# Performance work log

Measured on AMD Instinct MI355X. Metric: run time of the kernel, lower is better.

## Reference

```python
import jax, jax.numpy as jnp
import numpy as np
import math

N, B, S = 2048, 4, 1024
SFZ, IFZ, H, A = 384, 256, 8, 64
LN_EPS = 1e-5


def setup_inputs() -> dict:
    key = jax.random.key(0)
    ks = jax.random.split(key, 12)
    x = jax.random.normal(ks[0], (N, IFZ), dtype=jnp.float32)
    emb = jax.random.normal(ks[1], (B, S, SFZ), dtype=jnp.float32)
    mask = jax.random.randint(ks[2], (B, S), 0, 2).astype(bool)
    batch = jnp.sort(jax.random.randint(ks[3], (N,), 0, B)).astype(jnp.int64)
    sc = 1.0 / math.sqrt(IFZ)
    scs = 1.0 / math.sqrt(SFZ)
    Wq = jax.random.normal(ks[4], (IFZ, H * A), dtype=jnp.float32) * sc
    Wk = jax.random.normal(ks[5], (SFZ, H * A), dtype=jnp.float32) * scs
    Wv = jax.random.normal(ks[6], (SFZ, H * A), dtype=jnp.float32) * scs
    Wg = jax.random.normal(ks[7], (IFZ, H * A), dtype=jnp.float32) * sc
    bg = jnp.zeros((H * A,), dtype=jnp.float32)
    Wback = jax.random.normal(ks[8], (H * A, IFZ), dtype=jnp.float32) / math.sqrt(H * A)
    bback = jnp.zeros((IFZ,), dtype=jnp.float32)
    gamma = jnp.ones((IFZ,), dtype=jnp.float32)
    beta = jnp.zeros((IFZ,), dtype=jnp.float32)
    return {"x": x, "packed_sequence_emb": emb, "packed_sequence_mask": mask,
            "batch": batch, "Wq": Wq, "Wk": Wk, "Wv": Wv, "Wg": Wg, "bg": bg,
            "Wback": Wback, "bback": bback, "gamma": gamma, "beta": beta}


def _masked_softmax(scores, mask):
    # scores: [N,S,H], mask: [N,S,1] bool; softmax over S with padded entries zeroed
    neg = jnp.finfo(scores.dtype).min
    s = jnp.where(mask, scores, neg)
    s = s - jnp.max(s, axis=1, keepdims=True)
    e = jnp.exp(s) * mask
    return e / (jnp.sum(e, axis=1, keepdims=True) + 1e-9)


def reference(x, packed_sequence_emb, packed_sequence_mask, batch,
              Wq, Wk, Wv, Wg, bg, Wback, bback, gamma, beta):
    scale = math.sqrt(A)
    q = (x @ Wq).reshape(N, H, A)                               # [N,H,A]
    k = (packed_sequence_emb @ Wk).reshape(B, S, H, A)          # [B,S,H,A]
    v = (packed_sequence_emb @ Wv).reshape(B, S, H, A)
    # scores per (node, candidate-batch), then gather node's own batch entry;
    # avoids materializing k[batch] of shape [N,S,H,A]
    scores_all = jnp.einsum('nha,bsha->nbsh', q, k) / scale     # [N,B,S,H]
    idx = batch[:, None, None, None].astype(jnp.int32)
    scores = jnp.take_along_axis(scores_all, idx, axis=1)[:, 0]  # [N,S,H]
    bmask = packed_sequence_mask[batch][..., None]               # [N,S,1]
    w = _masked_softmax(scores, bmask)                           # [N,S,H]
    feat_all = jnp.einsum('nsh,bsha->nbha', w, v)                # [N,B,H,A]
    feat = jnp.take_along_axis(feat_all, idx, axis=1)[:, 0]      # [N,H,A]
    gate = jax.nn.sigmoid(x @ Wg + bg).reshape(N, H, A)
    new = (gate * feat).reshape(N, H * A) @ Wback + bback        # [N,IFZ]
    y = math.sqrt(2.0) * x + new
    mu = jnp.mean(y, axis=-1, keepdims=True)
    var = jnp.mean((y - mu) ** 2, axis=-1, keepdims=True)
    out = (y - mu) * jax.lax.rsqrt(var + LN_EPS) * gamma + beta
    seq_aa_logits = jnp.sum(scores[..., :2], axis=-1)            # [N,S]
    return out, seq_aa_logits
```

## Files before the change

### kernel.cpp

```cpp
#include <hip/hip_runtime.h>
#include <hip/hip_bf16.h>

#define NND 2048
#define BBATCH 4
#define SS 1024
#define SFZ 384
#define IFZ 256
#define HH 8
#define AA 64
#define HA 512
#define ABLK 12
#define NGRP 4
#define NSPL 8

typedef __attribute__((ext_vector_type(8))) short bf16x8;
typedef __attribute__((ext_vector_type(4))) float f32x4;
typedef __attribute__((ext_vector_type(2))) unsigned int u32x2;

__device__ __forceinline__ unsigned short f2bf(float f) {
    union { float f; unsigned u; } a; a.f = f;
    unsigned r = a.u + 0x7fffu + ((a.u >> 16) & 1u);
    return (unsigned short)(r >> 16);
}
__device__ __forceinline__ float bf2f(unsigned short u) {
    return __uint_as_float((unsigned)u << 16);
}

__device__ __forceinline__ bf16x8 cvt8(const float* __restrict__ p) {
    const float4 f0 = *(const float4*)p;
    const float4 f1 = *(const float4*)(p + 4);
    bf16x8 o;
    o[0] = (short)f2bf(f0.x); o[1] = (short)f2bf(f0.y);
    o[2] = (short)f2bf(f0.z); o[3] = (short)f2bf(f0.w);
    o[4] = (short)f2bf(f1.x); o[5] = (short)f2bf(f1.y);
    o[6] = (short)f2bf(f1.z); o[7] = (short)f2bf(f1.w);
    return o;
}

__device__ __forceinline__ bf16x8 gld16(const unsigned short* p) {
    bf16x8 r;
    asm volatile("global_load_dwordx4 %0, %1, off" : "=&v"(r) : "v"(p));
    return r;
}
__device__ __forceinline__ f32x4 gldf4(const float* p) {
    f32x4 r;
    asm volatile("global_load_dwordx4 %0, %1, off" : "=&v"(r) : "v"(p));
    return r;
}
__device__ __forceinline__ u32x2 gld8(const unsigned short* p) {
    u32x2 r;
    asm volatile("global_load_dwordx2 %0, %1, off" : "=&v"(r) : "v"(p));
    return r;
}
#define VMWAIT0() do { \
    asm volatile("s_waitcnt vmcnt(0)" ::: "memory"); \
    __builtin_amdgcn_sched_barrier(0); \
} while (0)

__device__ __forceinline__ void tile_transpose(
    const float* __restrict__ src, unsigned short* __restrict__ dst,
    int K, int N, int kt, int nt, int t)
{
    __shared__ unsigned short tile[64][65];
    const int k0 = kt * 64, n0 = nt * 64;
    const int tr = t >> 6, tc = t & 63;
    #pragma unroll
    for (int r = 0; r < 16; ++r)
        tile[tr + r*4][tc] = f2bf(src[(size_t)(k0 + tr + r*4) * N + n0 + tc]);
    __syncthreads();
    #pragma unroll
    for (int r = 0; r < 16; ++r)
        dst[(size_t)(n0 + tr + r*4) * K + k0 + tc] = tile[tc][tr + r*4];
}

__global__ __launch_bounds__(256) void prep_kernel(
    const float* __restrict__ Wk, const float* __restrict__ Wv,
    const float* __restrict__ Wq, const float* __restrict__ Wg,
    const float* __restrict__ Wback,
    const void* __restrict__ mask_raw, const void* __restrict__ batch_raw,
    unsigned short* __restrict__ WkT, unsigned short* __restrict__ WvT,
    unsigned short* __restrict__ WqT, unsigned short* __restrict__ WgT,
    unsigned short* __restrict__ WbackT,
    float* __restrict__ mask_f, int* __restrict__ seg)
{
    const int bx = blockIdx.x, t = threadIdx.x;
    if (bx < 48)  { tile_transpose(Wk, WkT, SFZ, HA, bx/8, bx%8, t); return; }
    if (bx < 96)  { const int i = bx-48;  tile_transpose(Wv, WvT, SFZ, HA, i/8, i%8, t); return; }
    if (bx < 128) { const int i = bx-96;  tile_transpose(Wq, WqT, IFZ, HA, i/8, i%8, t); return; }
    if (bx < 160) { const int i = bx-128; tile_transpose(Wg, WgT, IFZ, HA, i/8, i%8, t); return; }
    if (bx < 192) { const int i = bx-160; tile_transpose(Wback, WbackT, HA, IFZ, i/4, i%4, t); return; }
    __shared__ int fl[4];
    __shared__ int fb;
    __shared__ int cnt[4];
    if (t < 4) { fl[t] = 0; cnt[t] = 0; }
    if (t == 0) fb = 0;
    __syncthreads();
    const unsigned char*  mb = (const unsigned char*)mask_raw;
    const unsigned short* mh = (const unsigned short*)mask_raw;
    const unsigned int*   mw = (const unsigned int*)mask_raw;
    int f0 = 0, f1 = 0, f2 = 0, f3 = 0;
    for (int i = t; i < 2048; i += 256) {
        unsigned short h = mh[i];
        if (h == 0x3f80u) f0 = 1;
        if ((i & 1) == 0 && h != 0) f1 = 1;
    }
    for (int i = t; i < 4096; i += 256)
        if ((i & 3) != 0 && mb[i] != 0) f2 = 1;
    for (int i = t; i < 1024; i += 256)
        if ((i & 1) != 0 && mw[i] != 0) f3 = 1;
    const int* bw = (const int*)batch_raw;
    int f4 = 0;
    for (int i = t + 1; i < 2048; i += 256)
        if (bw[i] < bw[i-1]) f4 = 1;
    if (f0) atomicOr(&fl[0], 1);
    if (f1) atomicOr(&fl[1], 1);
    if (f2) atomicOr(&fl[2], 1);
    if (f3) atomicOr(&fl[3], 1);
    if (f4) atomicOr(&fb, 1);
    __syncthreads();
    int mode;
    if (fl[0])      mode = fl[1] ? 1 : 0;
    else if (fl[2]) mode = 2;
    else if (fl[3]) mode = 3;
    else            mode = 4;
    for (int s = t; s < BBATCH*SS; s += 256) {
        int m;
        switch (mode) {
            case 0:  m = (mw[s]   != 0); break;
            case 1:  m = (mh[s]   != 0); break;
            case 2:  m = (mb[s]   != 0); break;
            case 3:  m = (mw[s]   != 0); break;
            default: m = (mw[2*s] != 0); break;
        }
        mask_f[s] = m ? 1.0f : 0.0f;
    }
    const int b64 = fb;
    for (int i = t; i < NND; i += 256) {
        const int bv = (b64 ? bw[2*i] : bw[i]) & 3;
        atomicAdd(&cnt[bv], 1);
    }
    __syncthreads();
    if (t == 0) {
        int s = 0;
        for (int b = 0; b < 4; ++b) { seg[2*b] = s; s += cnt[b]; seg[2*b+1] = s; }
    }
}

__global__ __launch_bounds__(256, 2) void proj_mfma(
    const float* __restrict__ emb, const float* __restrict__ x,
    const unsigned short* __restrict__ WkT, const unsigned short* __restrict__ WvT,
    const unsigned short* __restrict__ WqT, const unsigned short* __restrict__ WgT,
    const float* __restrict__ bg,
    unsigned short* __restrict__ k_blk, unsigned short* __restrict__ vT_bf,
    unsigned short* __restrict__ q_bf, float* __restrict__ gate_ws)
{
    __shared__ unsigned short v_l[16][520];
    const int t = threadIdx.x, w = t >> 6, lane = t & 63;
    const int m16 = lane & 15, quad = lane >> 4;
    const int bx = blockIdx.x;
    if (bx < 256) {
        const int r0 = bx * 16;
        const int b = r0 >> 10, srow = r0 & (SS - 1);
        const float* ap = emb + (size_t)(r0 + m16) * SFZ + quad * 8;
        bf16x8 af[12];
        #pragma unroll
        for (int j = 0; j < 12; ++j) af[j] = cvt8(ap + j * 32);
        #pragma unroll
        for (int tensor = 0; tensor < 2; ++tensor) {
            const unsigned short* Wt = tensor ? WvT : WkT;
            #pragma unroll
            for (int g = 0; g < 2; ++g) {
                const int n0g = w * 128 + g * 64;
                const unsigned short* bp0 = Wt + (size_t)(n0g +  0 + m16) * SFZ + quad * 8;
                const unsigned short* bp1 = Wt + (size_t)(n0g + 16 + m16) * SFZ + quad * 8;
                const unsigned short* bp2 = Wt + (size_t)(n0g + 32 + m16) * SFZ + quad * 8;
                const unsigned short* bp3 = Wt + (size_t)(n0g + 48 + m16) * SFZ + quad * 8;
                f32x4 a0 = (f32x4){0.f, 0.f, 0.f, 0.f};
                f32x4 a1 = a0, a2 = a0, a3 = a0;
                bf16x8 wb[24];
                #pragma unroll
                for (int j = 0; j < 6; ++j) {
                    wb[j*4+0] = gld16(bp0 + j * 32);
                    wb[j*4+1] = gld16(bp1 + j * 32);
                    wb[j*4+2] = gld16(bp2 + j * 32);
                    wb[j*4+3] = gld16(bp3 + j * 32);
                }
                VMWAIT0();
                #pragma unroll
                for (int j = 0; j < 6; ++j) {
                    a0 = __builtin_amdgcn_mfma_f32_16x16x32_bf16(af[j], wb[j*4+0], a0, 0, 0, 0);
                    a1 = __builtin_amdgcn_mfma_f32_16x16x32_bf16(af[j], wb[j*4+1], a1, 0, 0, 0);
                    a2 = __builtin_amdgcn_mfma_f32_16x16x32_bf16(af[j], wb[j*4+2], a2, 0, 0, 0);
                    a3 = __builtin_amdgcn_mfma_f32_16x16x32_bf16(af[j], wb[j*4+3], a3, 0, 0, 0);
                }
                #pragma unroll
                for (int j = 6; j < 12; ++j) {
                    wb[(j-6)*4+0] = gld16(bp0 + j * 32);
                    wb[(j-6)*4+1] = gld16(bp1 + j * 32);
                    wb[(j-6)*4+2] = gld16(bp2 + j * 32);
                    wb[(j-6)*4+3] = gld16(bp3 + j * 32);
                }
                VMWAIT0();
                #pragma unroll
                for (int j = 6; j < 12; ++j) {
                    a0 = __builtin_amdgcn_mfma_f32_16x16x32_bf16(af[j], wb[(j-6)*4+0], a0, 0, 0, 0);
                    a1 = __builtin_amdgcn_mfma_f32_16x16x32_bf16(af[j], wb[(j-6)*4+1], a1, 0, 0, 0);
                    a2 = __builtin_amdgcn_mfma_f32_16x16x32_bf16(af[j], wb[(j-6)*4+2], a2, 0, 0, 0);
                    a3 = __builtin_amdgcn_mfma_f32_16x16x32_bf16(af[j], wb[(j-6)*4+3], a3, 0, 0, 0);
                }
                f32x4 dd[4] = {a0, a1, a2, a3};
                if (tensor == 0) {
                    #pragma unroll
                    for (int u = 0; u < 4; ++u) {
                        const int n0 = n0g + u * 16;
                        const int head = n0 >> 6, coff = (n0 & 63) + m16;
                        unsigned short* kb = k_blk + (((size_t)(b * HH + head)) * SS) * 64 + coff;
                        #pragma unroll
                        for (int r = 0; r < 4; ++r)
                            kb[(size_t)(srow + quad * 4 + r) * 64] = f2bf(dd[u][r]);
                    }
                } else {
                    #pragma unroll
                    for (int u = 0; u < 4; ++u) {
                        const int c0 = n0g + u * 16 + m16;
                        #pragma unroll
                        for (int r = 0; r < 4; ++r)
                            v_l[quad * 4 + r][c0] = f2bf(dd[u][r]);
                    }
                }
            }
        }
        __syncthreads();
        for (int c = t; c < HA; c += 256) {
            unsigned short tmp[16];
            #pragma unroll
            for (int s = 0; s < 16; ++s) tmp[s] = v_l[s][c];
            unsigned short* dst = vT_bf + ((size_t)b * HA + c) * SS + srow;
            *(uint4*)dst       = ((const uint4*)tmp)[0];
            *(uint4*)(dst + 8) = ((const uint4*)tmp)[1];
        }
    } else {
        const int i = bx - 256;
        const int r0 = (i >> 1) * 16;
        const int half = i & 1;
        const float* ap = x + (size_t)(r0 + m16) * IFZ + quad * 8;
        bf16x8 af[8];
        #pragma unroll
        for (int j = 0; j < 8; ++j) af[j] = cvt8(ap + j * 32);
        const int n0b = half * 256 + w * 64;
        #pragma unroll
        for (int tensor = 0; tensor < 2; ++tensor) {
            const unsigned short* Wt = tensor ? WgT : WqT;
            const unsigned short* bp0 = Wt + (size_t)(n0b +  0 + m16) * IFZ + quad * 8;
            const unsigned short* bp1 = Wt + (size_t)(n0b + 16 + m16) * IFZ + quad * 8;
            const unsigned short* bp2 = Wt + (size_t)(n0b + 32 + m16) * IFZ + quad * 8;
            const unsigned short* bp3 = Wt + (size_t)(n0b + 48 + m16) * IFZ + quad * 8;
            bf16x8 wb[32];
            #pragma unroll
            for (int j = 0; j < 8; ++j) {
                wb[j*4+0] = gld16(bp0 + j * 32);
                wb[j*4+1] = gld16(bp1 + j * 32);
                wb[j*4+2] = gld16(bp2 + j * 32);
                wb[j*4+3] = gld16(bp3 + j * 32);
            }
            VMWAIT0();
            f32x4 a0 = (f32x4){0.f, 0.f, 0.f, 0.f};
            f32x4 a1 = a0, a2 = a0, a3 = a0;
            #pragma unroll
            for (int j = 0; j < 8; ++j) {
                a0 = __builtin_amdgcn_mfma_f32_16x16x32_bf16(af[j], wb[j*4+0], a0, 0, 0, 0);
                a1 = __builtin_amdgcn_mfma_f32_16x16x32_bf16(af[j], wb[j*4+1], a1, 0, 0, 0);
                a2 = __builtin_amdgcn_mfma_f32_16x16x32_bf16(af[j], wb[j*4+2], a2, 0, 0, 0);
                a3 = __builtin_amdgcn_mfma_f32_16x16x32_bf16(af[j], wb[j*4+3], a3, 0, 0, 0);
            }
            f32x4 dd[4] = {a0, a1, a2, a3};
            if (tensor == 0) {
                #pragma unroll
                for (int u = 0; u < 4; ++u) {
                    const int n0 = n0b + u * 16;
                    #pragma unroll
                    for (int r = 0; r < 4; ++r)
                        q_bf[(size_t)(r0 + quad * 4 + r) * HA + n0 + m16] = f2bf(dd[u][r]);
                }
            } else {
                #pragma unroll
                for (int u = 0; u < 4; ++u) {
                    const int n0 = n0b + u * 16;
                    const float bgv = bg[n0 + m16];
                    #pragma unroll
                    for (int r = 0; r < 4; ++r)
                        gate_ws[(size_t)(r0 + quad * 4 + r) * HA + n0 + m16] =
                            1.f / (1.f + __expf(-(dd[u][r] + bgv)));
                }
            }
        }
    }
}

__global__ __launch_bounds__(256, 2) void attn_kernel(
    const unsigned short* __restrict__ k_blk, const unsigned short* __restrict__ vT_bf,
    const unsigned short* __restrict__ q_bf, const float* __restrict__ mask_f,
    const int* __restrict__ seg, unsigned short* __restrict__ part_O,
    float2* __restrict__ part_ml, float* __restrict__ out_logits)
{
    __shared__ unsigned short P_lds[4][16][136];
    __shared__ float raw[2][16][132];
    const int bid = blockIdx.x;
    const int xcd = bid & 7;
    const int b   = xcd >> 1;
    const int idx = (bid >> 3) * 2 + (xcd & 1);
    const int z    = idx & 15;
    const int xblk = idx >> 4;
    const int hz    = z >> 3;
    const int split = z & 7;
    const int nbase = seg[2*b] + xblk * (16 * NGRP);
    const int nend  = seg[2*b + 1];
    if (nbase >= nend) return;

    const int t = threadIdx.x;
    const int w = t >> 6, lane = t & 63;
    const int m16 = lane & 15, quad = lane >> 4;
    const int h = hz * 4 + w;
    const int s0 = split * 128;

    const unsigned short* kb = k_blk + ((size_t)(b * HH + h)) * SS * 64;
    const unsigned short* vb = vT_bf + ((size_t)b * HA + h * AA) * SS;
    const unsigned short* qbase = q_bf + (size_t)h * AA + quad * 8;
    unsigned short (*Pw)[136] = P_lds[w];

    bf16x8 kf[16];
    #pragma unroll
    for (int st = 0; st < 8; ++st) {
        const unsigned short* kp = kb + (size_t)(s0 + st * 16 + m16) * 64 + quad * 8;
        kf[2*st]   = gld16(kp);
        kf[2*st+1] = gld16(kp + 32);
    }
    f32x4 mkv[8];
    #pragma unroll
    for (int st = 0; st < 8; ++st)
        mkv[st] = gldf4(mask_f + b * SS + s0 + st * 16 + quad * 4);
    int nq0 = nbase + m16; if (nq0 >= nend) nq0 = nend - 1;
    bf16x8 qc0 = gld16(qbase + (size_t)nq0 * HA);
    bf16x8 qc1 = gld16(qbase + (size_t)nq0 * HA + 32);
    VMWAIT0();
    unsigned bm = 0u;
    #pragma unroll
    for (int st = 0; st < 8; ++st)
        #pragma unroll
        for (int r = 0; r < 4; ++r)
            if (mkv[st][r] > 0.5f) bm |= (1u << (st * 4 + r));

    bf16x8 qn0 = qc0, qn1 = qc1;
    for (int g = 0; g < NGRP; ++g) {
        const int n0g = nbase + g * 16;
        if (n0g >= nend) break;
        const int nvalid = min(16, nend - n0g);

        f32x4 d[8];
        #pragma unroll
        for (int st = 0; st < 8; ++st) {
            f32x4 acc = (f32x4){0.f, 0.f, 0.f, 0.f};
            acc = __builtin_amdgcn_mfma_f32_16x16x32_bf16(kf[2*st],   qc0, acc, 0, 0, 0);
            acc = __builtin_amdgcn_mfma_f32_16x16x32_bf16(kf[2*st+1], qc1, acc, 0, 0, 0);
            #pragma unroll
            for (int r = 0; r < 4; ++r) acc[r] *= 0.125f;
            d[st] = acc;
        }
        bf16x8 vf[16];
        #pragma unroll
        for (int sub = 0; sub < 4; ++sub) {
            const unsigned short* vp0 = vb + (size_t)m16 * SS + s0 + sub * 32 + quad * 8;
            #pragma unroll
            for (int a = 0; a < 4; ++a)
                vf[sub*4+a] = gld16(vp0 + (size_t)(a * 16) * SS);
        }
        if (g + 1 < NGRP && nbase + (g + 1) * 16 < nend) {
            int nqn = nbase + (g + 1) * 16 + m16; if (nqn >= nend) nqn = nend - 1;
            qn0 = gld16(qbase + (size_t)nqn * HA);
            qn1 = gld16(qbase + (size_t)nqn * HA + 32);
        }
        __builtin_amdgcn_sched_barrier(0);

        if (hz == 0) {
            if (w < 2) {
                #pragma unroll
                for (int st = 0; st < 8; ++st)
                    *(float4*)&raw[w][m16][st * 16 + quad * 4] =
                        make_float4(d[st][0], d[st][1], d[st][2], d[st][3]);
            }
            __syncthreads();
            for (int i = t; i < 16 * 128; i += 256) {
                const int node = i >> 7, sp = i & 127;
                if (node < nvalid)
                    out_logits[(size_t)(n0g + node) * SS + s0 + sp] =
                        raw[0][node][sp] + raw[1][node][sp];
            }
            __syncthreads();
        }
        #pragma unroll
        for (int st = 0; st < 8; ++st)
            #pragma unroll
            for (int r = 0; r < 4; ++r)
                if (!((bm >> (st * 4 + r)) & 1u)) d[st][r] = -3.0e38f;
        float mx = -3.0e38f;
        #pragma unroll
        for (int st = 0; st < 8; ++st) {
            float a = fmaxf(fmaxf(d[st][0], d[st][1]), fmaxf(d[st][2], d[st][3]));
            mx = fmaxf(mx, a);
        }
        mx = fmaxf(mx, __shfl_xor(mx, 16));
        mx = fmaxf(mx, __shfl_xor(mx, 32));
        mx = fmaxf(mx, -1.0e30f);
        float cs = 0.f;
        #pragma unroll
        for (int st = 0; st < 8; ++st)
            #pragma unroll
            for (int r = 0; r < 4; ++r) {
                const float e = __expf(d[st][r] - mx);
                d[st][r] = e;
                cs += e;
            }
        cs += __shfl_xor(cs, 16);
        cs += __shfl_xor(cs, 32);
        #pragma unroll
        for (int st = 0; st < 8; ++st) {
            ushort4 pk;
            pk.x = f2bf(d[st][0]); pk.y = f2bf(d[st][1]);
            pk.z = f2bf(d[st][2]); pk.w = f2bf(d[st][3]);
            *(ushort4*)&Pw[m16][st * 16 + quad * 4] = pk;
        }
        bf16x8 pa[4];
        #pragma unroll
        for (int sub = 0; sub < 4; ++sub)
            pa[sub] = *(const bf16x8*)&Pw[m16][sub * 32 + quad * 8];
        VMWAIT0();
        f32x4 facc[4];
        #pragma unroll
        for (int a = 0; a < 4; ++a) facc[a] = (f32x4){0.f, 0.f, 0.f, 0.f};
        #pragma unroll
        for (int sub = 0; sub < 4; ++sub) {
            #pragma unroll
            for (int a = 0; a < 4; ++a)
                facc[a] = __builtin_amdgcn_mfma_f32_16x16x32_bf16(pa[sub], vf[sub*4+a], facc[a], 0, 0, 0);
        }
        unsigned short* po = part_O + (size_t)split * NND * HA;
        #pragma unroll
        for (int a = 0; a < 4; ++a)
            #pragma unroll
            for (int r = 0; r < 4; ++r) {
                const int row = quad * 4 + r;
                if (row < nvalid)
                    po[(size_t)(n0g + row) * HA + h * AA + a * 16 + m16] = f2bf(facc[a][r]);
            }
        if (quad == 0 && m16 < nvalid)
            part_ml[(size_t)split * NND * HH + (size_t)(n0g + m16) * HH + h] =
                make_float2(mx, cs);
        qc0 = qn0; qc1 = qn1;
    }
}

__global__ __launch_bounds__(256, 2) void back_ln_fused(
    const unsigned short* __restrict__ part_O, const float2* __restrict__ part_ml,
    const float* __restrict__ gate_ws, const unsigned short* __restrict__ WbackT,
    const float* __restrict__ x, const float* __restrict__ bback,
    const float* __restrict__ gamma, const float* __restrict__ beta,
    float* __restrict__ out)
{
    __shared__ float coef[NSPL][8][8];
    __shared__ unsigned short gf_l[8][520];
    __shared__ float nl[8][260];
    const int t = threadIdx.x, w = t >> 6, lane = t & 63;
    const int m16 = lane & 15, quad = lane >> 4;
    const int r0 = blockIdx.x * 8;
    if (t < 64) {
        const int row = t >> 3, h = t & 7, n = r0 + row;
        float2 ml[NSPL];
        #pragma unroll
        for (int s = 0; s < NSPL; ++s)
            ml[s] = part_ml[(size_t)s * NND * HH + (size_t)n * HH + h];
        float M = -3.0e38f;
        #pragma unroll
        for (int s = 0; s < NSPL; ++s) M = fmaxf(M, ml[s].x);
        float L = 0.f;
        float e[NSPL];
        #pragma unroll
        for (int s = 0; s < NSPL; ++s) { e[s] = __expf(ml[s].x - M); L += ml[s].y * e[s]; }
        const float invL = 1.f / (L + 1e-9f);
        #pragma unroll
        for (int s = 0; s < NSPL; ++s) coef[s][row][h] = e[s] * invL;
    }
    u32x2 pvv[4][NSPL];
    f32x4 gv[4];
    #pragma unroll
    for (int it = 0; it < 4; ++it) {
        const int i = (t + it * 256) * 4;
        const int row = i >> 9, c = i & (HA - 1);
        const int n = r0 + row;
        #pragma unroll
        for (int s = 0; s < NSPL; ++s)
            pvv[it][s] = gld8(&part_O[(size_t)s * NND * HA + (size_t)n * HA + c]);
        gv[it] = gldf4(&gate_ws[(size_t)n * HA + c]);
    }
    __syncthreads();
    VMWAIT0();
    #pragma unroll
    for (int it = 0; it < 4; ++it) {
        const int i = (t + it * 256) * 4;
        const int row = i >> 9, c = i & (HA - 1), h = c >> 6;
        float4 o = make_float4(0.f, 0.f, 0.f, 0.f);
        #pragma unroll
        for (int s = 0; s < NSPL; ++s) {
            const float cf = coef[s][row][h];
            o.x = fmaf(bf2f((unsigned short)(pvv[it][s][0] & 0xffffu)), cf, o.x);
            o.y = fmaf(bf2f((unsigned short)(pvv[it][s][0] >> 16)),     cf, o.y);
            o.z = fmaf(bf2f((unsigned short)(pvv[it][s][1] & 0xffffu)), cf, o.z);
            o.w = fmaf(bf2f((unsigned short)(pvv[it][s][1] >> 16)),     cf, o.w);
        }
        ushort4 ob;
        ob.x = f2bf(gv[it][0] * o.x); ob.y = f2bf(gv[it][1] * o.y);
        ob.z = f2bf(gv[it][2] * o.z); ob.w = f2bf(gv[it][3] * o.w);
        *(ushort4*)&gf_l[row][c] = ob;
    }
    __syncthreads();
    bf16x8 af[16];
    #pragma unroll
    for (int j = 0; j < 16; ++j)
        af[j] = *(const bf16x8*)&gf_l[m16 & 7][quad * 8 + j * 32];
    const unsigned short* bq0 = WbackT + (size_t)(w * 64 +  0 + m16) * HA + quad * 8;
    const unsigned short* bq1 = WbackT + (size_t)(w * 64 + 16 + m16) * HA + quad * 8;
    const unsigned short* bq2 = WbackT + (size_t)(w * 64 + 32 + m16) * HA + quad * 8;
    const unsigned short* bq3 = WbackT + (size_t)(w * 64 + 48 + m16) * HA + quad * 8;
    f32x4 a0 = (f32x4){0.f, 0.f, 0.f, 0.f};
    f32x4 a1 = a0, a2 = a0, a3 = a0;
    #pragma unroll
    for (int jb = 0; jb < 4; ++jb) {
        bf16x8 wb[16];
        #pragma unroll
        for (int j = 0; j < 4; ++j) {
            wb[j*4+0] = gld16(bq0 + (jb*4 + j) * 32);
            wb[j*4+1] = gld16(bq1 + (jb*4 + j) * 32);
            wb[j*4+2] = gld16(bq2 + (jb*4 + j) * 32);
            wb[j*4+3] = gld16(bq3 + (jb*4 + j) * 32);
        }
        VMWAIT0();
        #pragma unroll
        for (int j = 0; j < 4; ++j) {
            a0 = __builtin_amdgcn_mfma_f32_16x16x32_bf16(af[jb*4+j], wb[j*4+0], a0, 0, 0, 0);
            a1 = __builtin_amdgcn_mfma_f32_16x16x32_bf16(af[jb*4+j], wb[j*4+1], a1, 0, 0, 0);
            a2 = __builtin_amdgcn_mfma_f32_16x16x32_bf16(af[jb*4+j], wb[j*4+2], a2, 0, 0, 0);
            a3 = __builtin_amdgcn_mfma_f32_16x16x32_bf16(af[jb*4+j], wb[j*4+3], a3, 0, 0, 0);
        }
    }
    {
        f32x4 dd[4] = {a0, a1, a2, a3};
        #pragma unroll
        for (int u = 0; u < 4; ++u) {
            const int n0 = w * 64 + u * 16;
            const float bb = bback[n0 + m16];
            #pragma unroll
            for (int r = 0; r < 4; ++r) {
                const int rr = quad * 4 + r;
                if (rr < 8) nl[rr][n0 + m16] = dd[u][r] + bb;
            }
        }
    }
    __syncthreads();
    const int row = t >> 5, li = t & 31;
    const float* xr = x + (size_t)(r0 + row) * IFZ;
    float yv[8];
    float s1 = 0.f, s2 = 0.f;
    #pragma unroll
    for (int j = 0; j < 8; ++j) {
        const int c = li + j * 32;
        const float v = fmaf(1.41421356237309515f, xr[c], nl[row][c]);
        yv[j] = v; s1 += v; s2 += v * v;
    }
    #pragma unroll
    for (int off = 16; off >= 1; off >>= 1) {
        s1 += __shfl_xor(s1, off);
        s2 += __shfl_xor(s2, off);
    }
    const float mu  = s1 * (1.f / IFZ);
    const float var = s2 * (1.f / IFZ) - mu * mu;
    const float rv  = rsqrtf(var + 1e-5f);
    float* orow = out + (size_t)(r0 + row) * IFZ;
    #pragma unroll
    for (int j = 0; j < 8; ++j) {
        const int c = li + j * 32;
        orow[c] = (yv[j] - mu) * rv * gamma[c] + beta[c];
    }
}

extern "C" void kernel_launch(void* const* d_in, const int* in_sizes, int n_in,
                              void* d_out, int out_size, void* d_ws, size_t ws_size,
                              hipStream_t stream) {
    const float* x     = (const float*)d_in[0];
    const float* emb   = (const float*)d_in[1];
    const void*  mraw  = d_in[2];
    const void*  braw  = d_in[3];
    const float* Wq    = (const float*)d_in[4];
    const float* Wk    = (const float*)d_in[5];
    const float* Wv    = (const float*)d_in[6];
    const float* Wg    = (const float*)d_in[7];
    const float* bg    = (const float*)d_in[8];
    const float* Wback = (const float*)d_in[9];
    const float* bback = (const float*)d_in[10];
    const float* gamma = (const float*)d_in[11];
    const float* beta  = (const float*)d_in[12];

    char* ws = (char*)d_ws;
    const size_t MB = 1048576;
    size_t off = 0;
    float*          mask_f  = (float*)(ws + off);  off += 16384;
    int*            seg     = (int*)(ws + off);    off += 16384;
    unsigned short* WkT     = (unsigned short*)(ws + off); off += 393216;
    unsigned short* WvT     = (unsigned short*)(ws + off); off += 393216;
    unsigned short* WqT     = (unsigned short*)(ws + off); off += 262144;
    unsigned short* WgT     = (unsigned short*)(ws + off); off += 262144;
    unsigned short* WbackT  = (unsigned short*)(ws + off); off += 262144;
    unsigned short* k_blk   = (unsigned short*)(ws + off); off += 4*MB;
    unsigned short* vT_bf   = (unsigned short*)(ws + off); off += 4*MB;
    unsigned short* q_bf    = (unsigned short*)(ws + off); off += 2*MB;
    float*          gate_ws = (float*)(ws + off); off += 4*MB;
    unsigned short* part_O  = (unsigned short*)(ws + off); off += 16*MB;
    float2*         part_ml = (float2*)(ws + off); off += 1*MB;

    float* out        = (float*)d_out;
    float* out_logits = out + (size_t)NND * IFZ;

    hipLaunchKernelGGL(prep_kernel, dim3(193), dim3(256), 0, stream,
                       Wk, Wv, Wq, Wg, Wback, mraw, braw,
                       WkT, WvT, WqT, WgT, WbackT, mask_f, seg);
    hipLaunchKernelGGL(proj_mfma, dim3(512), dim3(256), 0, stream,
                       emb, x, WkT, WvT, WqT, WgT, bg, k_blk, vT_bf, q_bf, gate_ws);
    hipLaunchKernelGGL(attn_kernel, dim3(BBATCH * ABLK * 16), dim3(256), 0, stream,
                       k_blk, vT_bf, q_bf, mask_f, seg, part_O, part_ml, out_logits);
    hipLaunchKernelGGL(back_ln_fused, dim3(NND / 8), dim3(256), 0, stream,
                       part_O, part_ml, gate_ws, WbackT, x, bback, gamma, beta, out);
}
```

Before: 186.8 us.

## Move seq logits computation into dedicated extra blocks of attention kernel

Removes the LDS staging and two __syncthreads per group that hz==0 attention blocks used to write the head-0+head-1 logits. Instead, extra blocks appended to the grid recompute the head-0 and head-1 QK scores with MFMA and write the logits directly. This takes synchronization and extra work off the attention critical path and balances load across hz halves, at the cost of redundant QK compute and extra K/Q loads in 96 additional blocks.

```diff
diff --git a/kernel.cpp b/kernel.cpp
--- a/kernel.cpp
+++ b/kernel.cpp
@@ -12,6 +12,8 @@
 #define ABLK 12
 #define NGRP 4
 #define NSPL 8
+#define ATTN_BLKS (BBATCH * ABLK * 16)
+#define LOGIT_BLKS (BBATCH * ABLK * 2)
 
 typedef __attribute__((ext_vector_type(8))) short bf16x8;
 typedef __attribute__((ext_vector_type(4))) float f32x4;
@@ -304,8 +306,64 @@
     float2* __restrict__ part_ml, float* __restrict__ out_logits)
 {
     __shared__ unsigned short P_lds[4][16][136];
-    __shared__ float raw[2][16][132];
     const int bid = blockIdx.x;
+    const int t = threadIdx.x;
+    const int w = t >> 6, lane = t & 63;
+    const int m16 = lane & 15, quad = lane >> 4;
+
+    if (bid >= ATTN_BLKS) {
+        const int lid = bid - ATTN_BLKS;
+        const int b = lid / 24;
+        const int rem = lid % 24;
+        const int xblk = rem >> 1;
+        const int spair = rem & 1;
+        const int s0 = (spair * 4 + w) * 128;
+        const int nbase = seg[2*b] + xblk * 64;
+        const int nend  = seg[2*b + 1];
+        if (nbase >= nend) return;
+        const unsigned short* kb0 = k_blk + ((size_t)(b * HH + 0)) * SS * 64;
+        const unsigned short* kb1 = k_blk + ((size_t)(b * HH + 1)) * SS * 64;
+        bf16x8 k0[16], k1[16];
+        #pragma unroll
+        for (int st = 0; st < 8; ++st) {
+            const unsigned short* kp0 = kb0 + (size_t)(s0 + st * 16 + m16) * 64 + quad * 8;
+            const unsigned short* kp1 = kb1 + (size_t)(s0 + st * 16 + m16) * 64 + quad * 8;
+            k0[2*st]   = gld16(kp0);
+            k0[2*st+1] = gld16(kp0 + 32);
+            k1[2*st]   = gld16(kp1);
+            k1[2*st+1] = gld16(kp1 + 32);
+        }
+        VMWAIT0();
+        for (int g = 0; g < NGRP; ++g) {
+            const int n0g = nbase + g * 16;
+            if (n0g >= nend) break;
+            const int nvalid = min(16, nend - n0g);
+            int nq = n0g + m16; if (nq >= nend) nq = nend - 1;
+            const unsigned short* qp = q_bf + (size_t)nq * HA + quad * 8;
+            const bf16x8 q0a = gld16(qp);
+            const bf16x8 q0b = gld16(qp + 32);
+            const bf16x8 q1a = gld16(qp + 64);
+            const bf16x8 q1b = gld16(qp + 96);
+            VMWAIT0();
+            #pragma unroll
+            for (int st = 0; st < 8; ++st) {
+                f32x4 acc = (f32x4){0.f, 0.f, 0.f, 0.f};
+                acc = __builtin_amdgcn_mfma_f32_16x16x32_bf16(q0a, k0[2*st],   acc, 0, 0, 0);
+                acc = __builtin_amdgcn_mfma_f32_16x16x32_bf16(q0b, k0[2*st+1], acc, 0, 0, 0);
+                acc = __builtin_amdgcn_mfma_f32_16x16x32_bf16(q1a, k1[2*st],   acc, 0, 0, 0);
+                acc = __builtin_amdgcn_mfma_f32_16x16x32_bf16(q1b, k1[2*st+1], acc, 0, 0, 0);
+                #pragma unroll
+                for (int r = 0; r < 4; ++r) {
+                    const int row = quad * 4 + r;
+                    if (row < nvalid)
+                        out_logits[(size_t)(n0g + row) * SS + s0 + st * 16 + m16] =
+                            acc[r] * 0.125f;
+                }
+            }
+        }
+        return;
+    }
+
     const int xcd = bid & 7;
     const int b   = xcd >> 1;
     const int idx = (bid >> 3) * 2 + (xcd & 1);
@@ -317,9 +375,6 @@
     const int nend  = seg[2*b + 1];
     if (nbase >= nend) return;
 
-    const int t = threadIdx.x;
-    const int w = t >> 6, lane = t & 63;
-    const int m16 = lane & 15, quad = lane >> 4;
     const int h = hz * 4 + w;
     const int s0 = split * 128;
 
@@ -381,22 +436,6 @@
         }
         __builtin_amdgcn_sched_barrier(0);
 
-        if (hz == 0) {
-            if (w < 2) {
-                #pragma unroll
-                for (int st = 0; st < 8; ++st)
-                    *(float4*)&raw[w][m16][st * 16 + quad * 4] =
-                        make_float4(d[st][0], d[st][1], d[st][2], d[st][3]);
-            }
-            __syncthreads();
-            for (int i = t; i < 16 * 128; i += 256) {
-                const int node = i >> 7, sp = i & 127;
-                if (node < nvalid)
-                    out_logits[(size_t)(n0g + node) * SS + s0 + sp] =
-                        raw[0][node][sp] + raw[1][node][sp];
-            }
-            __syncthreads();
-        }
         #pragma unroll
         for (int st = 0; st < 8; ++st)
             #pragma unroll
@@ -633,7 +672,7 @@
                        WkT, WvT, WqT, WgT, WbackT, mask_f, seg);
     hipLaunchKernelGGL(proj_mfma, dim3(512), dim3(256), 0, stream,
                        emb, x, WkT, WvT, WqT, WgT, bg, k_blk, vT_bf, q_bf, gate_ws);
-    hipLaunchKernelGGL(attn_kernel, dim3(BBATCH * ABLK * 16), dim3(256), 0, stream,
+    hipLaunchKernelGGL(attn_kernel, dim3(ATTN_BLKS + LOGIT_BLKS), dim3(256), 0, stream,
                        k_blk, vT_bf, q_bf, mask_f, seg, part_O, part_ml, out_logits);
     hipLaunchKernelGGL(back_ln_fused, dim3(NND / 8), dim3(256), 0, stream,
                        part_O, part_ml, gate_ws, WbackT, x, bback, gamma, beta, out);
```

Result: faster. 181.1 us (-3.1%).
